# Performance work log

Hardware: AMD Instinct MI355X
Metric: run time of the kernel (lower is better)

The kernel has to match this reference:

```python
import jax, jax.numpy as jnp
import numpy as np

B, CQ, CVK, L, H = 4, 256, 256, 2048, 8
D = CVK // H  # depth per head = 32
EPS = 1e-5    # BatchNorm eps


def setup_inputs() -> dict:
    key = jax.random.key(0)
    ks = jax.random.split(key, 32)
    n = lambda i, s, sc=1.0: jax.random.normal(ks[i], s, dtype=jnp.float32) * sc
    u = lambda i, s: jax.random.uniform(ks[i], s, dtype=jnp.float32, minval=0.5, maxval=1.5)
    inp = {
        'v': n(0, (B, CVK, L)), 'k': n(1, (B, CVK, L)), 'q': n(2, (B, CQ, L)),
        # trainable positional encodings (pe_q: image_shape_q, pe_vk: image_shape_vk)
        'pe_q': n(3, (CQ, L)), 'pe_vk': n(4, (CVK, L)),
        # W_query / W_key / W_value: Conv1d(kernel=1) weight [out,in] + bias, then BatchNorm1d (eval mode)
        'wq': n(5, (CVK, CQ), 0.05), 'bq': n(6, (CVK,), 0.05),
        'gq': 1.0 + n(7, (CVK,), 0.1), 'betaq': n(8, (CVK,), 0.1), 'mq': n(9, (CVK,), 0.1), 'varq': u(10, (CVK,)),
        'wk': n(11, (CVK, CVK), 0.05), 'bk': n(12, (CVK,), 0.05),
        'gk': 1.0 + n(13, (CVK,), 0.1), 'betak': n(14, (CVK,), 0.1), 'mk': n(15, (CVK,), 0.1), 'vark': u(16, (CVK,)),
        'wv': n(17, (CVK, CVK), 0.05), 'bv': n(18, (CVK,), 0.05),
        'gv': 1.0 + n(19, (CVK,), 0.1), 'betav': n(20, (CVK,), 0.1), 'mv': n(21, (CVK,), 0.1), 'varv': u(22, (CVK,)),
        # out_proj (zero-init in original; randomized here so gradients are non-trivial)
        'wo': n(23, (CQ, CVK), 0.05), 'bo': n(24, (CQ,), 0.05),
    }
    return inp


def _conv1(x, w, b):  # 1x1 conv == channel matmul: [b,c,l] -> [b,o,l]
    return jnp.einsum('oc,bcl->bol', w, x) + b[None, :, None]


def _bn(x, g, beta, mean, var):  # eval-mode BatchNorm1d over channel dim
    scale = g / jnp.sqrt(var + EPS)
    return (x - mean[:, None]) * scale[:, None] + beta[:, None]


def _mha(v, k, q, pe_q, pe_vk, wq, bq, gq, betaq, mq, varq,
         wk, bk, gk, betak, mk, vark, wv, bv, gv, betav, mv, varv, wo, bo):
    q_orig = q
    b = q.shape[0]
    vv = v + pe_vk[None]
    kk = k + pe_vk[None]
    qq = q + pe_q[None]
    qp = _bn(_conv1(qq, wq, bq), gq, betaq, mq, varq)   # [b, CVK, L]
    kp = _bn(_conv1(kk, wk, bk), gk, betak, mk, vark)
    vp = _bn(_conv1(vv, wv, bv), gv, betav, mv, varv)
    # split heads: [b, H, D, L]
    qh = qp.reshape(b, H, D, -1)
    kh = kp.reshape(b, H, D, -1)
    vh = vp.reshape(b, H, D, -1)
    # scaled dot-product attention over sequence dim (l: query pos, m: key pos)
    scores = jnp.einsum('bhdl,bhdm->bhlm', qh, kh) / jnp.sqrt(jnp.float32(D))
    p = jax.nn.softmax(scores, axis=-1)
    a = jnp.einsum('bhlm,bhdm->bhdl', p, vh)            # [b, H, D, L]
    a = a.reshape(b, H * D, -1)                          # [b, CVK, L]
    out = _conv1(a, wo, bo)                              # [b, CQ, L]
    return q_orig + out


def reference(v, k, q, pe_q, pe_vk, wq, bq, gq, betaq, mq, varq,
              wk, bk, gk, betak, mk, vark, wv, bv, gv, betav, mv, varv, wo, bo):
    return _mha(v, k, q, pe_q, pe_vk, wq, bq, gq, betaq, mq, varq,
                wk, bk, gk, betak, mk, vark, wv, bv, gv, betav, mv, varv, wo, bo)
```

## Files before the change

kernel.cpp:

```cpp
#include <hip/hip_runtime.h>
#include <hip/hip_bf16.h>

#define BB 4
#define CC 256
#define LL 2048
#define HH 8
#define DD 32
#define EPSV 1e-5f

typedef __bf16 bf16x8 __attribute__((ext_vector_type(8)));
typedef __bf16 bf16x4 __attribute__((ext_vector_type(4)));
typedef __bf16 bf16x2 __attribute__((ext_vector_type(2)));
typedef float  f32x4  __attribute__((ext_vector_type(4)));
typedef float  f32x16 __attribute__((ext_vector_type(16)));
typedef unsigned int u32x4 __attribute__((ext_vector_type(4)));

static __device__ __forceinline__ unsigned pkbf(float lo, float hi) {
    bf16x2 p; p[0] = (__bf16)lo; p[1] = (__bf16)hi;
    return __builtin_bit_cast(unsigned, p);
}

__global__ __launch_bounds__(512) void qkv_gemm_kernel(
    const float* __restrict__ qin, const float* __restrict__ kin,
    const float* __restrict__ vin,
    const float* __restrict__ peq, const float* __restrict__ pevk,
    const float* __restrict__ wq, const float* __restrict__ bq,
    const float* __restrict__ gq, const float* __restrict__ betaq,
    const float* __restrict__ mq, const float* __restrict__ varq,
    const float* __restrict__ wk, const float* __restrict__ bk,
    const float* __restrict__ gk, const float* __restrict__ betak,
    const float* __restrict__ mk, const float* __restrict__ vark,
    const float* __restrict__ wv, const float* __restrict__ bv,
    const float* __restrict__ gv, const float* __restrict__ betav,
    const float* __restrict__ mv, const float* __restrict__ varv,
    __bf16* __restrict__ qTo, __bf16* __restrict__ kTo, __bf16* __restrict__ vNo,
    float qscale)
{
    __shared__ __align__(16) __bf16 Wl[64][136];
    __shared__ __align__(16) __bf16 Xl[128][136];
    __bf16 (*Tl)[72] = (__bf16(*)[72])Xl;

    const int z = blockIdx.z;
    const int which = z >> 2;
    const int b = z & 3;
    const float* X    = which==0 ? qin : (which==1 ? kin : vin);
    const float* pe   = which==0 ? peq : pevk;
    const float* W    = which==0 ? wq  : (which==1 ? wk  : wv);
    const float* bia  = which==0 ? bq  : (which==1 ? bk  : bv);
    const float* gam  = which==0 ? gq  : (which==1 ? gk  : gv);
    const float* bet  = which==0 ? betaq : (which==1 ? betak : betav);
    const float* mea  = which==0 ? mq  : (which==1 ? mk  : mv);
    const float* var  = which==0 ? varq : (which==1 ? vark : varv);
    const float extra = (which==0) ? qscale : 1.0f;

    const int lt = blockIdx.x * 128;
    const int ot = blockIdx.y * 64;
    const int t  = threadIdx.x;
    const int wvi = t >> 6;
    const int wm = wvi >> 2;
    const int wn = wvi & 3;
    const int l  = t & 63;
    const int lq = l & 15;
    const int g  = l >> 4;

    f32x4 acc[2][2];
    #pragma unroll
    for (int mi = 0; mi < 2; ++mi)
        #pragma unroll
        for (int ni = 0; ni < 2; ++ni) acc[mi][ni] = (f32x4){0.f,0.f,0.f,0.f};

    for (int ks = 0; ks < 2; ++ks) {
        __syncthreads();
        #pragma unroll
        for (int i = 0; i < 4; ++i) {
            const int idx = i * 512 + t;
            const int row = idx >> 5;
            const int ch  = idx & 31;
            const int o   = ot + row;
            const float sc = gam[o] * rsqrtf(var[o] + EPSV) * extra;
            const float4 w4 = *(const float4*)&W[(size_t)o * CC + ks * 128 + ch * 4];
            bf16x4 wb;
            wb[0] = (__bf16)(w4.x * sc); wb[1] = (__bf16)(w4.y * sc);
            wb[2] = (__bf16)(w4.z * sc); wb[3] = (__bf16)(w4.w * sc);
            *(bf16x4*)&Wl[row][ch * 4] = wb;
        }
        #pragma unroll
        for (int i = 0; i < 2; ++i) {
            const int slot = i * 512 + t;
            const int lp = slot & 63;
            const int co = slot >> 6;
            const float* xp = &X[(size_t)(b * CC + ks * 128 + co * 8) * LL + lt + lp * 2];
            const float* pp = &pe[(size_t)(ks * 128 + co * 8) * LL + lt + lp * 2];
            bf16x8 lo, hi;
            #pragma unroll
            for (int j = 0; j < 8; ++j) {
                const float2 a = *(const float2*)&xp[(size_t)j * LL];
                const float2 p = *(const float2*)&pp[(size_t)j * LL];
                lo[j] = (__bf16)(a.x + p.x);
                hi[j] = (__bf16)(a.y + p.y);
            }
            *(bf16x8*)&Xl[lp * 2    ][co * 8] = lo;
            *(bf16x8*)&Xl[lp * 2 + 1][co * 8] = hi;
        }
        __syncthreads();

        #pragma unroll
        for (int kk = 0; kk < 4; ++kk) {
            bf16x8 af[2], bfr[2];
            #pragma unroll
            for (int mi = 0; mi < 2; ++mi)
                af[mi] = *(const bf16x8*)&Wl[wm * 32 + mi * 16 + lq][kk * 32 + g * 8];
            #pragma unroll
            for (int ni = 0; ni < 2; ++ni)
                bfr[ni] = *(const bf16x8*)&Xl[wn * 32 + ni * 16 + lq][kk * 32 + g * 8];
            #pragma unroll
            for (int mi = 0; mi < 2; ++mi)
                #pragma unroll
                for (int ni = 0; ni < 2; ++ni)
                    acc[mi][ni] = __builtin_amdgcn_mfma_f32_16x16x32_bf16(
                        af[mi], bfr[ni], acc[mi][ni], 0, 0, 0);
        }
    }

    float bb[2][4];
    #pragma unroll
    for (int mi = 0; mi < 2; ++mi) {
        const int o4 = ot + wm * 32 + mi * 16 + g * 4;
        const float4 b4 = *(const float4*)&bia[o4];
        const float4 g4 = *(const float4*)&gam[o4];
        const float4 v4 = *(const float4*)&var[o4];
        const float4 m4 = *(const float4*)&mea[o4];
        const float4 t4 = *(const float4*)&bet[o4];
        const float bs[4] = {b4.x,b4.y,b4.z,b4.w};
        const float gs[4] = {g4.x,g4.y,g4.z,g4.w};
        const float vs[4] = {v4.x,v4.y,v4.z,v4.w};
        const float ms[4] = {m4.x,m4.y,m4.z,m4.w};
        const float ts[4] = {t4.x,t4.y,t4.z,t4.w};
        #pragma unroll
        for (int r = 0; r < 4; ++r) {
            const float sc = gs[r] * rsqrtf(vs[r] + EPSV);
            bb[mi][r] = ((bs[r] - ms[r]) * sc + ts[r]) * extra;
        }
    }

    if (which < 2) {
        __bf16* outT = which==0 ? qTo : kTo;
        __syncthreads();
        #pragma unroll
        for (int mi = 0; mi < 2; ++mi) {
            #pragma unroll
            for (int ni = 0; ni < 2; ++ni) {
                bf16x4 pv;
                #pragma unroll
                for (int r = 0; r < 4; ++r) pv[r] = (__bf16)(acc[mi][ni][r] + bb[mi][r]);
                *(bf16x4*)&Tl[wn * 32 + ni * 16 + lq][wm * 32 + mi * 16 + g * 4] = pv;
            }
        }
        __syncthreads();
        #pragma unroll
        for (int i = 0; i < 2; ++i) {
            const int idx = i * 512 + t;
            const int lrow = idx >> 3, ch = idx & 7;
            *(bf16x8*)&outT[(size_t)(b * LL + lt + lrow) * CC + ot + ch * 8] =
                *(const bf16x8*)&Tl[lrow][ch * 8];
        }
    } else {
        #pragma unroll
        for (int mi = 0; mi < 2; ++mi) {
            #pragma unroll
            for (int ni = 0; ni < 2; ++ni) {
                const int col = lt + wn * 32 + ni * 16 + lq;
                #pragma unroll
                for (int r = 0; r < 4; ++r) {
                    const int o = ot + wm * 32 + mi * 16 + g * 4 + r;
                    vNo[(size_t)(b * CC + o) * LL + col] = (__bf16)(acc[mi][ni][r] + bb[mi][r]);
                }
            }
        }
    }
}

__global__ __launch_bounds__(256) void attn_mfma_kernel(
    const __bf16* __restrict__ qT, const __bf16* __restrict__ kT,
    const __bf16* __restrict__ vN, __bf16* __restrict__ aT)
{
    __shared__ __align__(16) __bf16 KB[2][128 * 32];
    __shared__ __align__(16) __bf16 VB[2][32 * 128];

    const int qb = blockIdx.x;
    const int h  = blockIdx.y;
    const int b  = blockIdx.z;
    const int t  = threadIdx.x;
    const int w  = t >> 6;
    const int l  = t & 63;
    const int lq = l & 31;
    const int hi = l >> 5;

    const int q0 = qb * 128 + w * 32;

    const __bf16* qrow = qT + ((size_t)(b * LL) + q0 + lq) * CC + h * DD;
    const bf16x8 qf0 = *(const bf16x8*)&qrow[hi * 8];
    const bf16x8 qf1 = *(const bf16x8*)&qrow[16 + hi * 8];

    const __bf16* kTb = kT + (size_t)(b * LL) * CC + h * DD;
    const __bf16* vNb = vN + ((size_t)(b * CC) + h * DD) * LL;

    const int s0 = t, s1 = 256 + t;
    const int sk0 = s0 >> 2, sp0 = s0 & 3;
    const int sk1 = s1 >> 2, sp1 = s1 & 3;
    const int sd0 = s0 >> 4, sv0 = s0 & 15;
    const int sd1 = s1 >> 4, sv1 = s1 & 15;
    const int kw0 = sk0 * 32 + (sp0 ^ ((sk0 >> 1) & 3)) * 8;
    const int kw1 = sk1 * 32 + (sp1 ^ ((sk1 >> 1) & 3)) * 8;
    const int vw0 = sd0 * 128 + (sv0 ^ (sd0 & 7)) * 8;
    const int vw1 = sd1 * 128 + (sv1 ^ (sd1 & 7)) * 8;

    bf16x8 kr0, kr1, vr0, vr1;
    #define LOADREGS(KT0) \
        kr0 = *(const bf16x8*)&kTb[(size_t)((KT0) + sk0) * CC + sp0 * 8]; \
        kr1 = *(const bf16x8*)&kTb[(size_t)((KT0) + sk1) * CC + sp1 * 8]; \
        vr0 = *(const bf16x8*)&vNb[(size_t)sd0 * LL + (KT0) + sv0 * 8];   \
        vr1 = *(const bf16x8*)&vNb[(size_t)sd1 * LL + (KT0) + sv1 * 8];
    #define WRITEBUF(BUF) \
        *(bf16x8*)&KB[BUF][kw0] = kr0; *(bf16x8*)&KB[BUF][kw1] = kr1; \
        *(bf16x8*)&VB[BUF][vw0] = vr0; *(bf16x8*)&VB[BUF][vw1] = vr1;

    LOADREGS(0)
    WRITEBUF(0)
    LOADREGS(128)

    f32x16 O;
    #pragma unroll
    for (int r = 0; r < 16; ++r) O[r] = 0.f;
    float ssum = 0.f;

    const int NT = LL / 128;
    for (int it = 0; it < NT; ++it) {
        const int buf = it & 1;
        __syncthreads();
        const __bf16* KBb = KB[buf];
        const __bf16* VBb = VB[buf];

        #pragma unroll
        for (int kb = 0; kb < 128; kb += 32) {
            const int key = kb + lq;
            const int ksw = (key >> 1) & 3;
            f32x16 S;
            #pragma unroll
            for (int r = 0; r < 16; ++r) S[r] = 0.f;
            {
                const bf16x8 kf0 = *(const bf16x8*)&KBb[key * 32 + ((hi    ) ^ ksw) * 8];
                const bf16x8 kf1 = *(const bf16x8*)&KBb[key * 32 + ((2 + hi) ^ ksw) * 8];
                __builtin_amdgcn_s_setprio(1);
                S = __builtin_amdgcn_mfma_f32_32x32x16_bf16(kf0, qf0, S, 0, 0, 0);
                S = __builtin_amdgcn_mfma_f32_32x32x16_bf16(kf1, qf1, S, 0, 0, 0);
                __builtin_amdgcn_s_setprio(0);
            }
            float e[16];
            #pragma unroll
            for (int r = 0; r < 16; ++r) e[r] = __builtin_amdgcn_exp2f(S[r]);
            float s = 0.f;
            #pragma unroll
            for (int r = 0; r < 16; r += 4) s += (e[r] + e[r+1]) + (e[r+2] + e[r+3]);
            ssum += s;
            unsigned a[8];
            #pragma unroll
            for (int i = 0; i < 8; ++i) a[i] = pkbf(e[2*i], e[2*i+1]);
            #pragma unroll
            for (int c = 0; c < 2; ++c) {
                unsigned w0 = a[4*c+0], w1 = a[4*c+1], w2 = a[4*c+2], w3 = a[4*c+3];
                asm volatile("v_permlane32_swap_b32 %0, %1" : "+v"(w0), "+v"(w2));
                asm volatile("v_permlane32_swap_b32 %0, %1" : "+v"(w1), "+v"(w3));
                u32x4 pv4 = {w0, w1, w2, w3};
                const bf16x8 pf = __builtin_bit_cast(bf16x8, pv4);
                const int slot = (kb >> 3) + 2 * c + hi;
                const bf16x8 vf = *(const bf16x8*)&VBb[lq * 128 + (slot ^ (lq & 7)) * 8];
                __builtin_amdgcn_s_setprio(1);
                O = __builtin_amdgcn_mfma_f32_32x32x16_bf16(vf, pf, O, 0, 0, 0);
                __builtin_amdgcn_s_setprio(0);
            }
        }

        if (it + 1 < NT) { WRITEBUF(buf ^ 1) }
        if (it + 2 < NT) { LOADREGS((it + 2) * 128) }
    }
    #undef LOADREGS
    #undef WRITEBUF

    ssum += __shfl_xor(ssum, 32);
    const float inv = 1.f / ssum;

    __bf16* arow = aT + ((size_t)(b * LL) + q0 + lq) * CC + h * DD;
    #pragma unroll
    for (int gi = 0; gi < 4; ++gi) {
        bf16x4 ov;
        #pragma unroll
        for (int r = 0; r < 4; ++r) ov[r] = (__bf16)(O[4*gi + r] * inv);
        *(bf16x4*)&arow[8 * gi + 4 * hi] = ov;
    }
}

__global__ __launch_bounds__(256) void outproj_kernel(
    const float* __restrict__ W, const __bf16* __restrict__ X,
    const float* __restrict__ bias, const float* __restrict__ resid,
    float* __restrict__ outF)
{
    __shared__ __align__(16) __bf16 Wl[64][136];
    __shared__ __align__(16) __bf16 Xl[64][136];

    const int lt = blockIdx.x * 64;
    const int ot = blockIdx.y * 64;
    const int b  = blockIdx.z;
    const int t  = threadIdx.x;
    const int wvi = t >> 6;
    const int wm = wvi >> 1;
    const int wn = wvi & 1;
    const int l  = t & 63;
    const int lq = l & 15;
    const int g  = l >> 4;

    f32x4 acc[2][2];
    #pragma unroll
    for (int mi = 0; mi < 2; ++mi)
        #pragma unroll
        for (int ni = 0; ni < 2; ++ni) acc[mi][ni] = (f32x4){0.f,0.f,0.f,0.f};

    for (int ks = 0; ks < 2; ++ks) {
        __syncthreads();
        #pragma unroll
        for (int i = 0; i < 8; ++i) {
            const int idx = i * 256 + t;
            const int row = idx >> 5;
            const int ch  = idx & 31;
            const float4 w4 = *(const float4*)&W[(size_t)(ot + row) * CC + ks * 128 + ch * 4];
            bf16x4 wb;
            wb[0] = (__bf16)w4.x; wb[1] = (__bf16)w4.y;
            wb[2] = (__bf16)w4.z; wb[3] = (__bf16)w4.w;
            *(bf16x4*)&Wl[row][ch * 4] = wb;
        }
        #pragma unroll
        for (int i = 0; i < 4; ++i) {
            const int idx = i * 256 + t;
            const int row = idx >> 4, ch = idx & 15;
            *(bf16x8*)&Xl[row][ch * 8] =
                *(const bf16x8*)&X[(size_t)(b * LL + lt + row) * CC + ks * 128 + ch * 8];
        }
        __syncthreads();

        #pragma unroll
        for (int kk = 0; kk < 4; ++kk) {
            bf16x8 af[2], bfr[2];
            #pragma unroll
            for (int mi = 0; mi < 2; ++mi)
                af[mi] = *(const bf16x8*)&Wl[wm * 32 + mi * 16 + lq][kk * 32 + g * 8];
            #pragma unroll
            for (int ni = 0; ni < 2; ++ni)
                bfr[ni] = *(const bf16x8*)&Xl[wn * 32 + ni * 16 + lq][kk * 32 + g * 8];
            #pragma unroll
            for (int mi = 0; mi < 2; ++mi)
                #pragma unroll
                for (int ni = 0; ni < 2; ++ni)
                    acc[mi][ni] = __builtin_amdgcn_mfma_f32_16x16x32_bf16(
                        af[mi], bfr[ni], acc[mi][ni], 0, 0, 0);
        }
    }

    #pragma unroll
    for (int mi = 0; mi < 2; ++mi) {
        const float4 b4 = *(const float4*)&bias[ot + wm * 32 + mi * 16 + g * 4];
        const float bb[4] = {b4.x, b4.y, b4.z, b4.w};
        #pragma unroll
        for (int ni = 0; ni < 2; ++ni) {
            const int col = lt + wn * 32 + ni * 16 + lq;
            #pragma unroll
            for (int r = 0; r < 4; ++r) {
                const int o = ot + wm * 32 + mi * 16 + g * 4 + r;
                const size_t a = (size_t)(b * CC + o) * LL + col;
                outF[a] = acc[mi][ni][r] + bb[r] + resid[a];
            }
        }
    }
}

extern "C" void kernel_launch(void* const* d_in, const int* in_sizes, int n_in,
                              void* d_out, int out_size, void* d_ws, size_t ws_size,
                              hipStream_t stream)
{
    const float* v     = (const float*)d_in[0];
    const float* k     = (const float*)d_in[1];
    const float* q     = (const float*)d_in[2];
    const float* pe_q  = (const float*)d_in[3];
    const float* pe_vk = (const float*)d_in[4];
    const float* wq    = (const float*)d_in[5];
    const float* bq    = (const float*)d_in[6];
    const float* gq    = (const float*)d_in[7];
    const float* betaq = (const float*)d_in[8];
    const float* mq    = (const float*)d_in[9];
    const float* varq  = (const float*)d_in[10];
    const float* wk    = (const float*)d_in[11];
    const float* bk    = (const float*)d_in[12];
    const float* gk    = (const float*)d_in[13];
    const float* betak = (const float*)d_in[14];
    const float* mk    = (const float*)d_in[15];
    const float* vark  = (const float*)d_in[16];
    const float* wv    = (const float*)d_in[17];
    const float* bv    = (const float*)d_in[18];
    const float* gv    = (const float*)d_in[19];
    const float* betav = (const float*)d_in[20];
    const float* mv    = (const float*)d_in[21];
    const float* varv  = (const float*)d_in[22];
    const float* wo    = (const float*)d_in[23];
    const float* bo    = (const float*)d_in[24];

    float* out = (float*)d_out;

    const size_t E = (size_t)BB * CC * LL;
    __bf16* qT  = (__bf16*)d_ws;
    __bf16* kT  = qT + E;
    __bf16* vN  = kT + E;
    __bf16* aT  = vN + E;

    const float qscale = 0.17677669529663687f * 1.4426950408889634f;

    hipLaunchKernelGGL(qkv_gemm_kernel, dim3(16, 4, 12), dim3(512), 0, stream,
                       q, k, v, pe_q, pe_vk,
                       wq, bq, gq, betaq, mq, varq,
                       wk, bk, gk, betak, mk, vark,
                       wv, bv, gv, betav, mv, varv,
                       qT, kT, vN, qscale);

    hipLaunchKernelGGL(attn_mfma_kernel, dim3(16, HH, BB), dim3(256), 0, stream,
                       qT, kT, vN, aT);

    hipLaunchKernelGGL(outproj_kernel, dim3(32, 4, 4), dim3(256), 0, stream,
                       wo, aT, bo, q, out);
}
```

Baseline: 65.11 us.

## Load full-K activation tile once and loop over all output channel tiles in QKV GEMM

The QKV projection kernel now gives each block a 64-column sequence tile with the full 256-channel reduction staged once in shared memory, then iterates over four 64-row output tiles. Previously each X tile was reloaded and re-converted from global fp32 for every output tile. Weights for the next output tile are prefetched into registers while the current one computes. The grid shrinks from 768 to 384 blocks, which lowers parallelism and adds per-iteration barriers, and shared memory per block grows.

```diff
diff --git a/kernel.cpp b/kernel.cpp
--- a/kernel.cpp
+++ b/kernel.cpp
@@ -36,9 +36,9 @@
     __bf16* __restrict__ qTo, __bf16* __restrict__ kTo, __bf16* __restrict__ vNo,
     float qscale)
 {
-    __shared__ __align__(16) __bf16 Wl[64][136];
-    __shared__ __align__(16) __bf16 Xl[128][136];
-    __bf16 (*Tl)[72] = (__bf16(*)[72])Xl;
+    __shared__ __align__(16) __bf16 Xl[64][264];
+    __shared__ __align__(16) __bf16 Wl[64][264];
+    __shared__ __align__(16) __bf16 Tl[64][72];
 
     const int z = blockIdx.z;
     const int which = z >> 2;
@@ -53,8 +53,7 @@
     const float* var  = which==0 ? varq : (which==1 ? vark : varv);
     const float extra = (which==0) ? qscale : 1.0f;
 
-    const int lt = blockIdx.x * 128;
-    const int ot = blockIdx.y * 64;
+    const int lt = blockIdx.x * 64;
     const int t  = threadIdx.x;
     const int wvi = t >> 6;
     const int wm = wvi >> 2;
@@ -63,117 +62,107 @@
     const int lq = l & 15;
     const int g  = l >> 4;
 
-    f32x4 acc[2][2];
-    #pragma unroll
-    for (int mi = 0; mi < 2; ++mi)
-        #pragma unroll
-        for (int ni = 0; ni < 2; ++ni) acc[mi][ni] = (f32x4){0.f,0.f,0.f,0.f};
-
-    for (int ks = 0; ks < 2; ++ks) {
+    float4 wreg[8];
+    const int wrow = t >> 6;
+    const int wch  = t & 63;
+    #pragma unroll
+    for (int i = 0; i < 8; ++i)
+        wreg[i] = *(const float4*)&W[(size_t)(i * 8 + wrow) * CC + wch * 4];
+
+    #pragma unroll
+    for (int i = 0; i < 2; ++i) {
+        const int slot = i * 512 + t;
+        const int lp = slot & 31;
+        const int co = slot >> 5;
+        const float* xp = &X[(size_t)(b * CC + co * 8) * LL + lt + lp * 2];
+        const float* pp = &pe[(size_t)(co * 8) * LL + lt + lp * 2];
+        bf16x8 lo, hi;
+        #pragma unroll
+        for (int j = 0; j < 8; ++j) {
+            const float2 a = *(const float2*)&xp[(size_t)j * LL];
+            const float2 p = *(const float2*)&pp[(size_t)j * LL];
+            lo[j] = (__bf16)(a.x + p.x);
+            hi[j] = (__bf16)(a.y + p.y);
+        }
+        *(bf16x8*)&Xl[lp * 2    ][co * 8] = lo;
+        *(bf16x8*)&Xl[lp * 2 + 1][co * 8] = hi;
+    }
+
+    for (int ot4 = 0; ot4 < 4; ++ot4) {
+        const int ot = ot4 * 64;
         __syncthreads();
-        #pragma unroll
-        for (int i = 0; i < 4; ++i) {
-            const int idx = i * 512 + t;
-            const int row = idx >> 5;
-            const int ch  = idx & 31;
-            const int o   = ot + row;
+
+        #pragma unroll
+        for (int i = 0; i < 8; ++i) {
+            const int o = ot + i * 8 + wrow;
             const float sc = gam[o] * rsqrtf(var[o] + EPSV) * extra;
-            const float4 w4 = *(const float4*)&W[(size_t)o * CC + ks * 128 + ch * 4];
             bf16x4 wb;
-            wb[0] = (__bf16)(w4.x * sc); wb[1] = (__bf16)(w4.y * sc);
-            wb[2] = (__bf16)(w4.z * sc); wb[3] = (__bf16)(w4.w * sc);
-            *(bf16x4*)&Wl[row][ch * 4] = wb;
-        }
-        #pragma unroll
-        for (int i = 0; i < 2; ++i) {
-            const int slot = i * 512 + t;
-            const int lp = slot & 63;
-            const int co = slot >> 6;
-            const float* xp = &X[(size_t)(b * CC + ks * 128 + co * 8) * LL + lt + lp * 2];
-            const float* pp = &pe[(size_t)(ks * 128 + co * 8) * LL + lt + lp * 2];
-            bf16x8 lo, hi;
-            #pragma unroll
-            for (int j = 0; j < 8; ++j) {
-                const float2 a = *(const float2*)&xp[(size_t)j * LL];
-                const float2 p = *(const float2*)&pp[(size_t)j * LL];
-                lo[j] = (__bf16)(a.x + p.x);
-                hi[j] = (__bf16)(a.y + p.y);
-            }
-            *(bf16x8*)&Xl[lp * 2    ][co * 8] = lo;
-            *(bf16x8*)&Xl[lp * 2 + 1][co * 8] = hi;
+            wb[0] = (__bf16)(wreg[i].x * sc); wb[1] = (__bf16)(wreg[i].y * sc);
+            wb[2] = (__bf16)(wreg[i].z * sc); wb[3] = (__bf16)(wreg[i].w * sc);
+            *(bf16x4*)&Wl[i * 8 + wrow][wch * 4] = wb;
+        }
+        if (ot4 < 3) {
+            #pragma unroll
+            for (int i = 0; i < 8; ++i)
+                wreg[i] = *(const float4*)&W[(size_t)(ot + 64 + i * 8 + wrow) * CC + wch * 4];
         }
         __syncthreads();
 
-        #pragma unroll
-        for (int kk = 0; kk < 4; ++kk) {
-            bf16x8 af[2], bfr[2];
-            #pragma unroll
-            for (int mi = 0; mi < 2; ++mi)
-                af[mi] = *(const bf16x8*)&Wl[wm * 32 + mi * 16 + lq][kk * 32 + g * 8];
-            #pragma unroll
-            for (int ni = 0; ni < 2; ++ni)
-                bfr[ni] = *(const bf16x8*)&Xl[wn * 32 + ni * 16 + lq][kk * 32 + g * 8];
-            #pragma unroll
-            for (int mi = 0; mi < 2; ++mi)
-                #pragma unroll
-                for (int ni = 0; ni < 2; ++ni)
-                    acc[mi][ni] = __builtin_amdgcn_mfma_f32_16x16x32_bf16(
-                        af[mi], bfr[ni], acc[mi][ni], 0, 0, 0);
-        }
-    }
-
-    float bb[2][4];
-    #pragma unroll
-    for (int mi = 0; mi < 2; ++mi) {
-        const int o4 = ot + wm * 32 + mi * 16 + g * 4;
-        const float4 b4 = *(const float4*)&bia[o4];
-        const float4 g4 = *(const float4*)&gam[o4];
-        const float4 v4 = *(const float4*)&var[o4];
-        const float4 m4 = *(const float4*)&mea[o4];
-        const float4 t4 = *(const float4*)&bet[o4];
-        const float bs[4] = {b4.x,b4.y,b4.z,b4.w};
-        const float gs[4] = {g4.x,g4.y,g4.z,g4.w};
-        const float vs[4] = {v4.x,v4.y,v4.z,v4.w};
-        const float ms[4] = {m4.x,m4.y,m4.z,m4.w};
-        const float ts[4] = {t4.x,t4.y,t4.z,t4.w};
-        #pragma unroll
-        for (int r = 0; r < 4; ++r) {
-            const float sc = gs[r] * rsqrtf(vs[r] + EPSV);
-            bb[mi][r] = ((bs[r] - ms[r]) * sc + ts[r]) * extra;
-        }
-    }
-
-    if (which < 2) {
-        __bf16* outT = which==0 ? qTo : kTo;
-        __syncthreads();
+        f32x4 acc[2];
+        acc[0] = (f32x4){0.f,0.f,0.f,0.f};
+        acc[1] = (f32x4){0.f,0.f,0.f,0.f};
+        #pragma unroll
+        for (int kk = 0; kk < 8; ++kk) {
+            const bf16x8 bfr = *(const bf16x8*)&Xl[wn * 16 + lq][kk * 32 + g * 8];
+            #pragma unroll
+            for (int mi = 0; mi < 2; ++mi) {
+                const bf16x8 af = *(const bf16x8*)&Wl[wm * 32 + mi * 16 + lq][kk * 32 + g * 8];
+                acc[mi] = __builtin_amdgcn_mfma_f32_16x16x32_bf16(af, bfr, acc[mi], 0, 0, 0);
+            }
+        }
+
+        float bb[2][4];
         #pragma unroll
         for (int mi = 0; mi < 2; ++mi) {
-            #pragma unroll
-            for (int ni = 0; ni < 2; ++ni) {
+            const int o4 = ot + wm * 32 + mi * 16 + g * 4;
+            const float4 b4 = *(const float4*)&bia[o4];
+            const float4 g4 = *(const float4*)&gam[o4];
+            const float4 v4 = *(const float4*)&var[o4];
+            const float4 m4 = *(const float4*)&mea[o4];
+            const float4 t4 = *(const float4*)&bet[o4];
+            const float bs[4] = {b4.x,b4.y,b4.z,b4.w};
+            const float gs[4] = {g4.x,g4.y,g4.z,g4.w};
+            const float vs[4] = {v4.x,v4.y,v4.z,v4.w};
+            const float ms[4] = {m4.x,m4.y,m4.z,m4.w};
+            const float ts[4] = {t4.x,t4.y,t4.z,t4.w};
+            #pragma unroll
+            for (int r = 0; r < 4; ++r) {
+                const float sc = gs[r] * rsqrtf(vs[r] + EPSV);
+                bb[mi][r] = ((bs[r] - ms[r]) * sc + ts[r]) * extra;
+            }
+        }
+
+        if (which < 2) {
+            __bf16* outT = which==0 ? qTo : kTo;
+            #pragma unroll
+            for (int mi = 0; mi < 2; ++mi) {
                 bf16x4 pv;
                 #pragma unroll
-                for (int r = 0; r < 4; ++r) pv[r] = (__bf16)(acc[mi][ni][r] + bb[mi][r]);
-                *(bf16x4*)&Tl[wn * 32 + ni * 16 + lq][wm * 32 + mi * 16 + g * 4] = pv;
-            }
-        }
-        __syncthreads();
-        #pragma unroll
-        for (int i = 0; i < 2; ++i) {
-            const int idx = i * 512 + t;
-            const int lrow = idx >> 3, ch = idx & 7;
+                for (int r = 0; r < 4; ++r) pv[r] = (__bf16)(acc[mi][r] + bb[mi][r]);
+                *(bf16x4*)&Tl[wn * 16 + lq][wm * 32 + mi * 16 + g * 4] = pv;
+            }
+            __syncthreads();
+            const int lrow = t >> 3, ch = t & 7;
             *(bf16x8*)&outT[(size_t)(b * LL + lt + lrow) * CC + ot + ch * 8] =
                 *(const bf16x8*)&Tl[lrow][ch * 8];
-        }
-    } else {
-        #pragma unroll
-        for (int mi = 0; mi < 2; ++mi) {
-            #pragma unroll
-            for (int ni = 0; ni < 2; ++ni) {
-                const int col = lt + wn * 32 + ni * 16 + lq;
+        } else {
+            #pragma unroll
+            for (int mi = 0; mi < 2; ++mi) {
+                const int col = lt + wn * 16 + lq;
                 #pragma unroll
                 for (int r = 0; r < 4; ++r) {
                     const int o = ot + wm * 32 + mi * 16 + g * 4 + r;
-                    vNo[(size_t)(b * CC + o) * LL + col] = (__bf16)(acc[mi][ni][r] + bb[mi][r]);
+                    vNo[(size_t)(b * CC + o) * LL + col] = (__bf16)(acc[mi][r] + bb[mi][r]);
                 }
             }
         }
@@ -422,7 +411,7 @@
 
     const float qscale = 0.17677669529663687f * 1.4426950408889634f;
 
-    hipLaunchKernelGGL(qkv_gemm_kernel, dim3(16, 4, 12), dim3(512), 0, stream,
+    hipLaunchKernelGGL(qkv_gemm_kernel, dim3(32, 1, 12), dim3(512), 0, stream,
                        q, k, v, pe_q, pe_vk,
                        wq, bq, gq, betaq, mq, varq,
                        wk, bk, gk, betak, mk, vark,
```

Result: slower. 67.52 us (+3.7%).

## Split attention key range in two and add a combine kernel

Applied to the files above, without the earlier changes.

Each attention block now handles only half of the key sequence, so twice as many blocks are launched, with an occupancy hint of 4 blocks per SIMD. Each block writes unnormalised fp32 partial outputs and partial softmax sums to a workspace. A new combine kernel adds the two halves, normalises, transposes through shared memory and writes the bf16 attention output. The aim is better GPU fill during attention. In exchange it costs an extra launch and a large fp32 round trip through global memory for the partial results.

```diff
diff --git a/kernel.cpp b/kernel.cpp
--- a/kernel.cpp
+++ b/kernel.cpp
@@ -180,23 +180,26 @@
     }
 }
 
-__global__ __launch_bounds__(256) void attn_mfma_kernel(
+__global__ __launch_bounds__(256, 4) void attn_mfma_kernel(
     const __bf16* __restrict__ qT, const __bf16* __restrict__ kT,
-    const __bf16* __restrict__ vN, __bf16* __restrict__ aT)
+    const __bf16* __restrict__ vN, float* __restrict__ Ow,
+    float* __restrict__ Sw)
 {
     __shared__ __align__(16) __bf16 KB[2][128 * 32];
     __shared__ __align__(16) __bf16 VB[2][32 * 128];
 
-    const int qb = blockIdx.x;
-    const int h  = blockIdx.y;
-    const int b  = blockIdx.z;
-    const int t  = threadIdx.x;
+    const int qb   = blockIdx.x;
+    const int h    = blockIdx.y >> 1;
+    const int half = blockIdx.y & 1;
+    const int b    = blockIdx.z;
+    const int t    = threadIdx.x;
     const int w  = t >> 6;
     const int l  = t & 63;
     const int lq = l & 31;
     const int hi = l >> 5;
 
     const int q0 = qb * 128 + w * 32;
+    const int kbase = half * 1024;
 
     const __bf16* qrow = qT + ((size_t)(b * LL) + q0 + lq) * CC + h * DD;
     const bf16x8 qf0 = *(const bf16x8*)&qrow[hi * 8];
@@ -225,16 +228,16 @@
         *(bf16x8*)&KB[BUF][kw0] = kr0; *(bf16x8*)&KB[BUF][kw1] = kr1; \
         *(bf16x8*)&VB[BUF][vw0] = vr0; *(bf16x8*)&VB[BUF][vw1] = vr1;
 
-    LOADREGS(0)
+    LOADREGS(kbase)
     WRITEBUF(0)
-    LOADREGS(128)
+    LOADREGS(kbase + 128)
 
     f32x16 O;
     #pragma unroll
     for (int r = 0; r < 16; ++r) O[r] = 0.f;
     float ssum = 0.f;
 
-    const int NT = LL / 128;
+    const int NT = 1024 / 128;
     for (int it = 0; it < NT; ++it) {
         const int buf = it & 1;
         __syncthreads();
@@ -282,22 +285,59 @@
         }
 
         if (it + 1 < NT) { WRITEBUF(buf ^ 1) }
-        if (it + 2 < NT) { LOADREGS((it + 2) * 128) }
+        if (it + 2 < NT) { LOADREGS(kbase + (it + 2) * 128) }
     }
     #undef LOADREGS
     #undef WRITEBUF
 
     ssum += __shfl_xor(ssum, 32);
-    const float inv = 1.f / ssum;
-
-    __bf16* arow = aT + ((size_t)(b * LL) + q0 + lq) * CC + h * DD;
+
+    float* orow = Ow + (size_t)(((b * HH + h) * 2 + half) * DD) * LL;
     #pragma unroll
     for (int gi = 0; gi < 4; ++gi) {
-        bf16x4 ov;
-        #pragma unroll
-        for (int r = 0; r < 4; ++r) ov[r] = (__bf16)(O[4*gi + r] * inv);
-        *(bf16x4*)&arow[8 * gi + 4 * hi] = ov;
-    }
+        #pragma unroll
+        for (int r = 0; r < 4; ++r) {
+            const int d = 8 * gi + 4 * hi + r;
+            orow[(size_t)d * LL + q0 + lq] = O[4 * gi + r];
+        }
+    }
+    if (l < 32)
+        Sw[(size_t)((b * HH + h) * 2 + half) * LL + q0 + lq] = ssum;
+}
+
+__global__ __launch_bounds__(256) void combine_kernel(
+    const float* __restrict__ Ow, const float* __restrict__ Sw,
+    __bf16* __restrict__ aT)
+{
+    __shared__ float invs[64];
+    __shared__ __align__(16) __bf16 Tl[64][40];
+
+    const int lt = blockIdx.x * 64;
+    const int h  = blockIdx.y;
+    const int b  = blockIdx.z;
+    const int t  = threadIdx.x;
+
+    if (t < 64) {
+        const float s0 = Sw[(size_t)((b * HH + h) * 2 + 0) * LL + lt + t];
+        const float s1 = Sw[(size_t)((b * HH + h) * 2 + 1) * LL + lt + t];
+        invs[t] = 1.f / (s0 + s1);
+    }
+    __syncthreads();
+
+    const float* O0 = Ow + (size_t)(((b * HH + h) * 2 + 0) * DD) * LL;
+    const float* O1 = Ow + (size_t)(((b * HH + h) * 2 + 1) * DD) * LL;
+    #pragma unroll
+    for (int i = 0; i < 8; ++i) {
+        const int idx = i * 256 + t;
+        const int d = idx >> 6, q = idx & 63;
+        const float v = (O0[(size_t)d * LL + lt + q] + O1[(size_t)d * LL + lt + q]) * invs[q];
+        Tl[q][d] = (__bf16)v;
+    }
+    __syncthreads();
+
+    const int q = t >> 2, dc = t & 3;
+    *(bf16x8*)&aT[((size_t)(b * LL) + lt + q) * CC + h * DD + dc * 8] =
+        *(const bf16x8*)&Tl[q][dc * 8];
 }
 
 __global__ __launch_bounds__(256) void outproj_kernel(
@@ -419,6 +459,8 @@
     __bf16* kT  = qT + E;
     __bf16* vN  = kT + E;
     __bf16* aT  = vN + E;
+    float*  Ow  = (float*)(aT + E);
+    float*  Sw  = Ow + 2 * E;
 
     const float qscale = 0.17677669529663687f * 1.4426950408889634f;
 
@@ -429,8 +471,11 @@
                        wv, bv, gv, betav, mv, varv,
                        qT, kT, vN, qscale);
 
-    hipLaunchKernelGGL(attn_mfma_kernel, dim3(16, HH, BB), dim3(256), 0, stream,
-                       qT, kT, vN, aT);
+    hipLaunchKernelGGL(attn_mfma_kernel, dim3(16, 16, BB), dim3(256), 0, stream,
+                       qT, kT, vN, Ow, Sw);
+
+    hipLaunchKernelGGL(combine_kernel, dim3(32, HH, BB), dim3(256), 0, stream,
+                       Ow, Sw, aT);
 
     hipLaunchKernelGGL(outproj_kernel, dim3(32, 4, 4), dim3(256), 0, stream,
                        wo, aT, bo, q, out);
```

Result: slower. 70.33 us (+8.0%).

## Software-pipeline attention QK/softmax/PV stages and remap blocks across XCDs

Applied to the files above, without the earlier changes.

Restructures the attention inner loop so that QK^T MFMAs for the next 32-key chunk are issued before the softmax and PV MFMAs of the previous chunk. This interleaves exp/pack work with matrix ops to hide MFMA latency. The next tile's shared-memory write and global prefetch now happen right after the barrier instead of at the end of the iteration. Blocks are remapped so that all q-blocks of the same (batch, head) land on the same XCD for L2 reuse of K/V, and launch bounds request two blocks per CU. The explicit setprio hints are dropped, and keeping four S tiles live raises register pressure.

```diff
diff --git a/kernel.cpp b/kernel.cpp
--- a/kernel.cpp
+++ b/kernel.cpp
@@ -180,16 +180,21 @@
     }
 }
 
-__global__ __launch_bounds__(256) void attn_mfma_kernel(
+__global__ __launch_bounds__(256, 2) void attn_mfma_kernel(
     const __bf16* __restrict__ qT, const __bf16* __restrict__ kT,
     const __bf16* __restrict__ vN, __bf16* __restrict__ aT)
 {
     __shared__ __align__(16) __bf16 KB[2][128 * 32];
     __shared__ __align__(16) __bf16 VB[2][32 * 128];
 
-    const int qb = blockIdx.x;
-    const int h  = blockIdx.y;
-    const int b  = blockIdx.z;
+    const int flat = blockIdx.x + 16 * (blockIdx.y + 8 * blockIdx.z);
+    const int xcd  = flat & 7;
+    const int ixc  = flat >> 3;
+    const int gidx = xcd + 8 * (ixc >> 4);
+    const int qb   = ixc & 15;
+    const int h    = gidx & 7;
+    const int b    = gidx >> 3;
+
     const int t  = threadIdx.x;
     const int w  = t >> 6;
     const int l  = t & 63;
@@ -233,59 +238,76 @@
     #pragma unroll
     for (int r = 0; r < 16; ++r) O[r] = 0.f;
     float ssum = 0.f;
+    f32x16 Z16;
+    #pragma unroll
+    for (int r = 0; r < 16; ++r) Z16[r] = 0.f;
+
+    #define QKC(kbv, S) { \
+        const int key_ = (kbv) + lq; \
+        const int ksw_ = (key_ >> 1) & 3; \
+        const bf16x8 kf0_ = *(const bf16x8*)&KBb[key_ * 32 + ((hi    ) ^ ksw_) * 8]; \
+        const bf16x8 kf1_ = *(const bf16x8*)&KBb[key_ * 32 + ((2 + hi) ^ ksw_) * 8]; \
+        S = __builtin_amdgcn_mfma_f32_32x32x16_bf16(kf0_, qf0, Z16, 0, 0, 0); \
+        S = __builtin_amdgcn_mfma_f32_32x32x16_bf16(kf1_, qf1, S, 0, 0, 0); }
+
+    #define SMC(S, P0, P1) { \
+        float e_[16]; \
+        _Pragma("unroll") \
+        for (int r = 0; r < 16; ++r) e_[r] = __builtin_amdgcn_exp2f(S[r]); \
+        float s_ = 0.f; \
+        _Pragma("unroll") \
+        for (int r = 0; r < 16; r += 4) s_ += (e_[r] + e_[r+1]) + (e_[r+2] + e_[r+3]); \
+        ssum += s_; \
+        unsigned a_[8]; \
+        _Pragma("unroll") \
+        for (int i = 0; i < 8; ++i) a_[i] = pkbf(e_[2*i], e_[2*i+1]); \
+        { unsigned w0_ = a_[0], w1_ = a_[1], w2_ = a_[2], w3_ = a_[3]; \
+          asm volatile("v_permlane32_swap_b32 %0, %1" : "+v"(w0_), "+v"(w2_)); \
+          asm volatile("v_permlane32_swap_b32 %0, %1" : "+v"(w1_), "+v"(w3_)); \
+          P0 = (u32x4){w0_, w1_, w2_, w3_}; } \
+        { unsigned w0_ = a_[4], w1_ = a_[5], w2_ = a_[6], w3_ = a_[7]; \
+          asm volatile("v_permlane32_swap_b32 %0, %1" : "+v"(w0_), "+v"(w2_)); \
+          asm volatile("v_permlane32_swap_b32 %0, %1" : "+v"(w1_), "+v"(w3_)); \
+          P1 = (u32x4){w0_, w1_, w2_, w3_}; } }
+
+    #define PVC(kbv, P0, P1) { \
+        const bf16x8 pf0_ = __builtin_bit_cast(bf16x8, P0); \
+        const bf16x8 vf0_ = *(const bf16x8*)&VBb[lq * 128 + ((((kbv) >> 3) + hi    ) ^ (lq & 7)) * 8]; \
+        O = __builtin_amdgcn_mfma_f32_32x32x16_bf16(vf0_, pf0_, O, 0, 0, 0); \
+        const bf16x8 pf1_ = __builtin_bit_cast(bf16x8, P1); \
+        const bf16x8 vf1_ = *(const bf16x8*)&VBb[lq * 128 + ((((kbv) >> 3) + 2 + hi) ^ (lq & 7)) * 8]; \
+        O = __builtin_amdgcn_mfma_f32_32x32x16_bf16(vf1_, pf1_, O, 0, 0, 0); }
 
     const int NT = LL / 128;
     for (int it = 0; it < NT; ++it) {
         const int buf = it & 1;
         __syncthreads();
+        if (it + 1 < NT) { WRITEBUF(buf ^ 1) }
+        if (it + 2 < NT) { LOADREGS((it + 2) * 128) }
+
         const __bf16* KBb = KB[buf];
         const __bf16* VBb = VB[buf];
 
-        #pragma unroll
-        for (int kb = 0; kb < 128; kb += 32) {
-            const int key = kb + lq;
-            const int ksw = (key >> 1) & 3;
-            f32x16 S;
-            #pragma unroll
-            for (int r = 0; r < 16; ++r) S[r] = 0.f;
-            {
-                const bf16x8 kf0 = *(const bf16x8*)&KBb[key * 32 + ((hi    ) ^ ksw) * 8];
-                const bf16x8 kf1 = *(const bf16x8*)&KBb[key * 32 + ((2 + hi) ^ ksw) * 8];
-                __builtin_amdgcn_s_setprio(1);
-                S = __builtin_amdgcn_mfma_f32_32x32x16_bf16(kf0, qf0, S, 0, 0, 0);
-                S = __builtin_amdgcn_mfma_f32_32x32x16_bf16(kf1, qf1, S, 0, 0, 0);
-                __builtin_amdgcn_s_setprio(0);
-            }
-            float e[16];
-            #pragma unroll
-            for (int r = 0; r < 16; ++r) e[r] = __builtin_amdgcn_exp2f(S[r]);
-            float s = 0.f;
-            #pragma unroll
-            for (int r = 0; r < 16; r += 4) s += (e[r] + e[r+1]) + (e[r+2] + e[r+3]);
-            ssum += s;
-            unsigned a[8];
-            #pragma unroll
-            for (int i = 0; i < 8; ++i) a[i] = pkbf(e[2*i], e[2*i+1]);
-            #pragma unroll
-            for (int c = 0; c < 2; ++c) {
-                unsigned w0 = a[4*c+0], w1 = a[4*c+1], w2 = a[4*c+2], w3 = a[4*c+3];
-                asm volatile("v_permlane32_swap_b32 %0, %1" : "+v"(w0), "+v"(w2));
-                asm volatile("v_permlane32_swap_b32 %0, %1" : "+v"(w1), "+v"(w3));
-                u32x4 pv4 = {w0, w1, w2, w3};
-                const bf16x8 pf = __builtin_bit_cast(bf16x8, pv4);
-                const int slot = (kb >> 3) + 2 * c + hi;
-                const bf16x8 vf = *(const bf16x8*)&VBb[lq * 128 + (slot ^ (lq & 7)) * 8];
-                __builtin_amdgcn_s_setprio(1);
-                O = __builtin_amdgcn_mfma_f32_32x32x16_bf16(vf, pf, O, 0, 0, 0);
-                __builtin_amdgcn_s_setprio(0);
-            }
-        }
-
-        if (it + 1 < NT) { WRITEBUF(buf ^ 1) }
-        if (it + 2 < NT) { LOADREGS((it + 2) * 128) }
+        f32x16 S0, S1, S2, S3;
+        u32x4 P0a, P0b, P1a, P1b, P2a, P2b, P3a, P3b;
+        QKC(0,  S0)
+        QKC(32, S1)
+        SMC(S0, P0a, P0b)
+        QKC(64, S2)
+        PVC(0,  P0a, P0b)
+        SMC(S1, P1a, P1b)
+        QKC(96, S3)
+        PVC(32, P1a, P1b)
+        SMC(S2, P2a, P2b)
+        PVC(64, P2a, P2b)
+        SMC(S3, P3a, P3b)
+        PVC(96, P3a, P3b)
     }
     #undef LOADREGS
     #undef WRITEBUF
+    #undef QKC
+    #undef SMC
+    #undef PVC
 
     ssum += __shfl_xor(ssum, 32);
     const float inv = 1.f / ssum;
```

After: 60.53 us. -7.0%, faster.
